# Kernel tuning notes

Hardware: AMD Instinct MI355X
Metric: run time of the kernel (lower is better)

The kernel has to match this reference:

```python
import jax, jax.numpy as jnp
import numpy as np

N = 100000
E = 1600000
C_IN = 128
H = 128
C_OUT = 128
DEPTH = 3
RATIO = 0.5
EPS = 1e-5


def gcn_conv(x, W, b, src, dst, mask, n):
    # PyG GCNConv: out = D^-1/2 (A+I) D^-1/2 (x @ W) + b, masked edges dropped
    h = x @ W  # [n, out]
    ew = mask.astype(h.dtype)  # [E]
    deg = 1.0 + jax.ops.segment_sum(ew, dst, num_segments=n)  # self-loop included
    dinv = jax.lax.rsqrt(deg)
    norm = dinv[src] * dinv[dst] * ew  # [E]
    agg = jax.ops.segment_sum(h[src] * norm[:, None], dst, num_segments=n)
    agg = agg + h * (1.0 / deg)[:, None]  # self-loop contribution
    return agg + b


def bn_train(x, g, beta):
    # BatchNorm1d training forward: biased variance over nodes
    m = jnp.mean(x, axis=0)
    v = jnp.mean((x - m) ** 2, axis=0)
    return (x - m) * jax.lax.rsqrt(v + EPS) * g + beta


def topk_pool(x, w, src, dst, mask, k):
    # score = tanh(x.w / ||w||); keep top-k nodes, relabel edges, mask invalid ones
    score = jnp.tanh((x * w).sum(-1) / jnp.sqrt((w * w).sum()))
    _, idx = jax.lax.top_k(score, k)
    n = x.shape[0]
    new_id = jnp.zeros((n,), jnp.int32).at[idx].set(jnp.arange(k, dtype=jnp.int32))
    kept = jnp.zeros((n,), bool).at[idx].set(True)
    mask2 = mask & kept[src] & kept[dst]
    return x[idx], new_id[src], new_id[dst], mask2, idx


def setup_inputs() -> dict:
    key = jax.random.key(0)
    ks = jax.random.split(key, 16)
    sc_in = 1.0 / np.sqrt(C_IN)
    sc_h = 1.0 / np.sqrt(H)
    sc_2h = 1.0 / np.sqrt(2 * H)
    return {
        "x": jax.random.normal(ks[0], (N, C_IN), jnp.float32),
        "edge_index": jax.random.randint(ks[1], (2, E), 0, N, dtype=jnp.int32),
        "in_W": jax.random.normal(ks[2], (C_IN, H), jnp.float32) * sc_in,
        "in_b": jnp.zeros((H,), jnp.float32),
        "dn_W": jax.random.normal(ks[3], (DEPTH, H, H), jnp.float32) * sc_h,
        "dn_b": jnp.zeros((DEPTH, H), jnp.float32),
        "dn_g": jnp.ones((DEPTH, H), jnp.float32),
        "dn_beta": jnp.zeros((DEPTH, H), jnp.float32),
        "pool_w": jax.random.normal(ks[4], (DEPTH, H), jnp.float32),
        "bot_W": jax.random.normal(ks[5], (H, H), jnp.float32) * sc_h,
        "bot_b": jnp.zeros((H,), jnp.float32),
        "up_W": jax.random.normal(ks[6], (DEPTH, 2 * H, H), jnp.float32) * sc_2h,
        "up_b": jnp.zeros((DEPTH, H), jnp.float32),
        "up_g": jnp.ones((DEPTH, H), jnp.float32),
        "up_beta": jnp.zeros((DEPTH, H), jnp.float32),
        "out_W": jax.random.normal(ks[7], (H, C_OUT), jnp.float32) * sc_h,
        "out_b": jnp.zeros((C_OUT,), jnp.float32),
    }


def reference(x, edge_index, in_W, in_b, dn_W, dn_b, dn_g, dn_beta, pool_w,
              bot_W, bot_b, up_W, up_b, up_g, up_beta, out_W, out_b):
    src, dst = edge_index[0], edge_index[1]
    mask = jnp.ones((src.shape[0],), bool)
    n = x.shape[0]
    x = gcn_conv(x, in_W, in_b, src, dst, mask, n)
    xs, stack = [], []
    for i in range(DEPTH):
        x = gcn_conv(x, dn_W[i], dn_b[i], src, dst, mask, n)
        x = jax.nn.relu(bn_train(x, dn_g[i], dn_beta[i]))
        xs.append(x)
        k = int(RATIO * n)
        x2, src2, dst2, mask2, idx = topk_pool(x, pool_w[i], src, dst, mask, k)
        stack.append((src, dst, mask, idx, n))
        x, src, dst, mask, n = x2, src2, dst2, mask2, k
    x = jax.nn.relu(gcn_conv(x, bot_W, bot_b, src, dst, mask, n))
    for i in range(DEPTH):
        psrc, pdst, pmask, idx, pn = stack[DEPTH - 1 - i]
        xf = jnp.zeros((pn, x.shape[1]), x.dtype).at[idx].set(x)  # unpool zero-scatter
        src, dst, mask, n = psrc, pdst, pmask, pn
        x = jnp.concatenate([xf, xs[DEPTH - 1 - i]], axis=1)  # [pn, 2H]
        x = gcn_conv(x, up_W[i], up_b[i], src, dst, mask, n)
        x = jax.nn.relu(bn_train(x, up_g[i], up_beta[i]))
    return gcn_conv(x, out_W, out_b, src, dst, mask, n)
```

## Files before the change

kernel.cpp:

```cpp
#include <hip/hip_runtime.h>

typedef unsigned long long ull;

#define N0_ 100000
#define N1_ 50000
#define N2_ 25000
#define N3_ 12500
#define EDG 1600000
#define CAP1 600000
#define CAP2 200000
#define CAP3 80000
#define RB 65536

struct Sel { ull prefix; int remaining; };


__global__ void sentinel_k(float* o, float v) { if (threadIdx.x == 0) o[0] = v; }

template <typename TA, typename TC, typename ACC>
__global__ __launch_bounds__(256) void matmul128(const TA* __restrict__ A,
    const float* __restrict__ W, const float* __restrict__ bias,
    TC* __restrict__ C, int n) {
  __shared__ float Al[64 * 33];
  __shared__ float Wl[32 * 128];
  int tid = threadIdx.x;
  int colb = tid & 31;
  int rg = tid >> 5;
  int row0 = blockIdx.x * 64;
  ACC acc[8][4];
#pragma unroll
  for (int r = 0; r < 8; ++r)
#pragma unroll
    for (int j = 0; j < 4; ++j) acc[r][j] = (ACC)0;
  for (int kt = 0; kt < 128; kt += 32) {
    for (int i = tid; i < 64 * 32; i += 256) {
      int r = i >> 5, kk = i & 31;
      int row = row0 + r;
      Al[r * 33 + kk] = (row < n) ? (float)A[(size_t)row * 128 + kt + kk] : 0.0f;
    }
    for (int i = tid; i < 32 * 128; i += 256) {
      int kk = i >> 7, c = i & 127;
      Wl[i] = W[(size_t)(kt + kk) * 128 + c];
    }
    __syncthreads();
#pragma unroll 4
    for (int kk = 0; kk < 32; ++kk) {
      ACC b0 = (ACC)Wl[kk * 128 + colb];
      ACC b1 = (ACC)Wl[kk * 128 + colb + 32];
      ACC b2 = (ACC)Wl[kk * 128 + colb + 64];
      ACC b3 = (ACC)Wl[kk * 128 + colb + 96];
#pragma unroll
      for (int r = 0; r < 8; ++r) {
        ACC a = (ACC)Al[(rg * 8 + r) * 33 + kk];
        acc[r][0] += a * b0; acc[r][1] += a * b1;
        acc[r][2] += a * b2; acc[r][3] += a * b3;
      }
    }
    __syncthreads();
  }
  ACC bb0 = 0, bb1 = 0, bb2 = 0, bb3 = 0;
  if (bias) {
    bb0 = (ACC)bias[colb]; bb1 = (ACC)bias[colb + 32];
    bb2 = (ACC)bias[colb + 64]; bb3 = (ACC)bias[colb + 96];
  }
  for (int r = 0; r < 8; ++r) {
    int row = row0 + rg * 8 + r;
    if (row < n) {
      size_t o = (size_t)row * 128 + colb;
      C[o] = (TC)(acc[r][0] + bb0); C[o + 32] = (TC)(acc[r][1] + bb1);
      C[o + 64] = (TC)(acc[r][2] + bb2); C[o + 96] = (TC)(acc[r][3] + bb3);
    }
  }
}

template <bool RELU>
__global__ __launch_bounds__(256) void agg_conv(const float* __restrict__ hp,
    const int* __restrict__ off, const int* __restrict__ csrc,
    const float* __restrict__ csrw,
    const double* __restrict__ dinv, const double* __restrict__ dgi,
    const float* __restrict__ bias, float* __restrict__ yp, int n) {
  const float4* __restrict__ h = (const float4*)hp;
  float4* __restrict__ y = (float4*)yp;
  int lane = threadIdx.x & 63;
  int c4 = lane & 31;
  int half = lane >> 5;
  int node = blockIdx.x * 4 + (threadIdx.x >> 6);
  if (node >= n) return;
  double di = dinv[node];
  double dg = dgi[node];
  double aX = 0, aY = 0, aZ = 0, aW = 0;
  int p0 = off[node], p1 = off[node + 1];
  int m = p1 - p0;
  int npair = m >> 1;
  int j = 0;
  for (; j + 8 <= npair; j += 8) {
    int e0 = p0 + 2 * j + half;
    int s0 = csrc[e0],      s1 = csrc[e0 + 2],  s2 = csrc[e0 + 4],  s3 = csrc[e0 + 6];
    int s4 = csrc[e0 + 8],  s5 = csrc[e0 + 10], s6 = csrc[e0 + 12], s7 = csrc[e0 + 14];
    double w0 = (double)csrw[e0],      w1 = (double)csrw[e0 + 2];
    double w2 = (double)csrw[e0 + 4],  w3 = (double)csrw[e0 + 6];
    double w4 = (double)csrw[e0 + 8],  w5 = (double)csrw[e0 + 10];
    double w6 = (double)csrw[e0 + 12], w7 = (double)csrw[e0 + 14];
    float4 v0 = h[(size_t)s0 * 32 + c4];
    float4 v1 = h[(size_t)s1 * 32 + c4];
    float4 v2 = h[(size_t)s2 * 32 + c4];
    float4 v3 = h[(size_t)s3 * 32 + c4];
    float4 v4 = h[(size_t)s4 * 32 + c4];
    float4 v5 = h[(size_t)s5 * 32 + c4];
    float4 v6 = h[(size_t)s6 * 32 + c4];
    float4 v7 = h[(size_t)s7 * 32 + c4];
    aX += (double)v0.x * w0; aY += (double)v0.y * w0;
    aZ += (double)v0.z * w0; aW += (double)v0.w * w0;
    aX += (double)v1.x * w1; aY += (double)v1.y * w1;
    aZ += (double)v1.z * w1; aW += (double)v1.w * w1;
    aX += (double)v2.x * w2; aY += (double)v2.y * w2;
    aZ += (double)v2.z * w2; aW += (double)v2.w * w2;
    aX += (double)v3.x * w3; aY += (double)v3.y * w3;
    aZ += (double)v3.z * w3; aW += (double)v3.w * w3;
    aX += (double)v4.x * w4; aY += (double)v4.y * w4;
    aZ += (double)v4.z * w4; aW += (double)v4.w * w4;
    aX += (double)v5.x * w5; aY += (double)v5.y * w5;
    aZ += (double)v5.z * w5; aW += (double)v5.w * w5;
    aX += (double)v6.x * w6; aY += (double)v6.y * w6;
    aZ += (double)v6.z * w6; aW += (double)v6.w * w6;
    aX += (double)v7.x * w7; aY += (double)v7.y * w7;
    aZ += (double)v7.z * w7; aW += (double)v7.w * w7;
  }
  for (; j + 4 <= npair; j += 4) {
    int e0 = p0 + 2 * j + half;
    int s0 = csrc[e0], s1 = csrc[e0 + 2], s2 = csrc[e0 + 4], s3 = csrc[e0 + 6];
    double w0 = (double)csrw[e0],     w1 = (double)csrw[e0 + 2];
    double w2 = (double)csrw[e0 + 4], w3 = (double)csrw[e0 + 6];
    float4 v0 = h[(size_t)s0 * 32 + c4];
    float4 v1 = h[(size_t)s1 * 32 + c4];
    float4 v2 = h[(size_t)s2 * 32 + c4];
    float4 v3 = h[(size_t)s3 * 32 + c4];
    aX += (double)v0.x * w0; aY += (double)v0.y * w0;
    aZ += (double)v0.z * w0; aW += (double)v0.w * w0;
    aX += (double)v1.x * w1; aY += (double)v1.y * w1;
    aZ += (double)v1.z * w1; aW += (double)v1.w * w1;
    aX += (double)v2.x * w2; aY += (double)v2.y * w2;
    aZ += (double)v2.z * w2; aW += (double)v2.w * w2;
    aX += (double)v3.x * w3; aY += (double)v3.y * w3;
    aZ += (double)v3.z * w3; aW += (double)v3.w * w3;
  }
  for (; j < npair; ++j) {
    int e = p0 + 2 * j + half;
    double w = (double)csrw[e];
    float4 v = h[(size_t)csrc[e] * 32 + c4];
    aX += (double)v.x * w; aY += (double)v.y * w;
    aZ += (double)v.z * w; aW += (double)v.w * w;
  }
  if ((m & 1) && half == 0) {
    int e = p1 - 1;
    double w = (double)csrw[e];
    float4 v = h[(size_t)csrc[e] * 32 + c4];
    aX += (double)v.x * w; aY += (double)v.y * w;
    aZ += (double)v.z * w; aW += (double)v.w * w;
  }
  double sX = aX + __shfl_xor(aX, 32);
  double sY = aY + __shfl_xor(aY, 32);
  double sZ = aZ + __shfl_xor(aZ, 32);
  double sW = aW + __shfl_xor(aW, 32);
  if (half == 0) {
    float4 hv = h[(size_t)node * 32 + c4];
    double bx = 0, by = 0, bz = 0, bw = 0;
    if (bias) {
      bx = (double)bias[c4 * 4 + 0]; by = (double)bias[c4 * 4 + 1];
      bz = (double)bias[c4 * 4 + 2]; bw = (double)bias[c4 * 4 + 3];
    }
    double rx = sX * di + (double)hv.x * dg + bx;
    double ry = sY * di + (double)hv.y * dg + by;
    double rz = sZ * di + (double)hv.z * dg + bz;
    double rw = sW * di + (double)hv.w * dg + bw;
    if (RELU) {
      rx = rx > 0.0 ? rx : 0.0; ry = ry > 0.0 ? ry : 0.0;
      rz = rz > 0.0 ? rz : 0.0; rw = rw > 0.0 ? rw : 0.0;
    }
    y[(size_t)node * 32 + c4] = make_float4((float)rx, (float)ry, (float)rz, (float)rw);
  }
}

__global__ void count_deg(const int* __restrict__ dst, int m, int* __restrict__ cnt) {
  int e = blockIdx.x * 256 + threadIdx.x;
  if (e < m) atomicAdd(&cnt[dst[e]], 1);
}

__global__ void fin_deg(const int* __restrict__ cnt, double* __restrict__ dinv,
                        double* __restrict__ dgi, int n) {
  int i = blockIdx.x * 256 + threadIdx.x;
  if (i < n) {
    double d = 1.0 + (double)cnt[i];
    dinv[i] = 1.0 / sqrt(d);
    dgi[i] = 1.0 / d;
  }
}

__global__ __launch_bounds__(256) void scan_part(const int* __restrict__ in,
                                                 int* __restrict__ bsum, int n) {
  __shared__ int ts[256];
  int base = blockIdx.x * 1024 + threadIdx.x * 4;
  int s = 0;
#pragma unroll
  for (int j = 0; j < 4; ++j) { int i = base + j; if (i < n) s += in[i]; }
  ts[threadIdx.x] = s;
  __syncthreads();
  for (int d = 128; d > 0; d >>= 1) {
    if (threadIdx.x < d) ts[threadIdx.x] += ts[threadIdx.x + d];
    __syncthreads();
  }
  if (threadIdx.x == 0) bsum[blockIdx.x] = ts[0];
}

__global__ __launch_bounds__(256) void scan_bsum(int* __restrict__ bsum, int nb) {
  __shared__ int ls[256];
  int t = threadIdx.x;
  int v = (t < nb) ? bsum[t] : 0;
  ls[t] = v;
  __syncthreads();
  for (int d = 1; d < 256; d <<= 1) {
    int u = (t >= d) ? ls[t - d] : 0;
    __syncthreads();
    ls[t] += u;
    __syncthreads();
  }
  if (t < nb) bsum[t] = ls[t] - v;
}

__global__ __launch_bounds__(256) void scan_out(const int* __restrict__ in,
    const int* __restrict__ bsum, int* __restrict__ out, int n, int nb) {
  __shared__ int ts[256];
  int base = blockIdx.x * 1024 + threadIdx.x * 4;
  int loc[4];
  int s = 0;
#pragma unroll
  for (int j = 0; j < 4; ++j) {
    int i = base + j;
    int v = (i < n) ? in[i] : 0;
    loc[j] = s; s += v;
  }
  ts[threadIdx.x] = s;
  __syncthreads();
  int mine = s;
  for (int d = 1; d < 256; d <<= 1) {
    int u = (threadIdx.x >= d) ? ts[threadIdx.x - d] : 0;
    __syncthreads();
    ts[threadIdx.x] += u;
    __syncthreads();
  }
  int toff = bsum[blockIdx.x] + ts[threadIdx.x] - mine;
#pragma unroll
  for (int j = 0; j < 4; ++j) {
    int i = base + j;
    if (i < n) out[i] = toff + loc[j];
  }
  if (blockIdx.x == nb - 1 && threadIdx.x == 255) out[n] = bsum[blockIdx.x] + ts[255];
}

template <int MODE>
__device__ __forceinline__ int sel_flag(ull u, ull pref, int epre, int rem) {
  if (MODE == 1) return (u == pref) ? 1 : 0;
  return (u > pref || (u == pref && epre < rem)) ? 1 : 0;
}

template <int MODE>
__global__ __launch_bounds__(256) void fscan_part(const ull* __restrict__ keys,
    const int* __restrict__ eqpre, const Sel* __restrict__ sel,
    int* __restrict__ bsum, int n) {
  __shared__ int ts[256];
  ull pref = sel->prefix;
  int rem = sel->remaining;
  int base = blockIdx.x * 1024 + threadIdx.x * 4;
  int s = 0;
#pragma unroll
  for (int j = 0; j < 4; ++j) {
    int i = base + j;
    if (i < n) s += sel_flag<MODE>(keys[i], pref, (MODE == 2) ? eqpre[i] : 0, rem);
  }
  ts[threadIdx.x] = s;
  __syncthreads();
  for (int d = 128; d > 0; d >>= 1) {
    if (threadIdx.x < d) ts[threadIdx.x] += ts[threadIdx.x + d];
    __syncthreads();
  }
  if (threadIdx.x == 0) bsum[blockIdx.x] = ts[0];
}

__global__ __launch_bounds__(256) void fscan_out1(const ull* __restrict__ keys,
    const Sel* __restrict__ sel, const int* __restrict__ bsum,
    int* __restrict__ eqpre_out, int n) {
  __shared__ int ts[256];
  ull pref = sel->prefix;
  int base = blockIdx.x * 1024 + threadIdx.x * 4;
  int loc[4];
  int s = 0;
#pragma unroll
  for (int j = 0; j < 4; ++j) {
    int i = base + j;
    int v = (i < n) ? sel_flag<1>(keys[i], pref, 0, 0) : 0;
    loc[j] = s; s += v;
  }
  ts[threadIdx.x] = s;
  __syncthreads();
  int mine = s;
  for (int d = 1; d < 256; d <<= 1) {
    int u = (threadIdx.x >= d) ? ts[threadIdx.x - d] : 0;
    __syncthreads();
    ts[threadIdx.x] += u;
    __syncthreads();
  }
  int toff = bsum[blockIdx.x] + ts[threadIdx.x] - mine;
#pragma unroll
  for (int j = 0; j < 4; ++j) {
    int i = base + j;
    if (i < n) eqpre_out[i] = toff + loc[j];
  }
}

__global__ __launch_bounds__(256) void fscan_out2(const ull* __restrict__ keys,
    const int* __restrict__ eqpre, const Sel* __restrict__ sel,
    const int* __restrict__ bsum, int* __restrict__ knid, int* __restrict__ idx,
    int n) {
  __shared__ int ts[256];
  ull pref = sel->prefix;
  int rem = sel->remaining;
  int base = blockIdx.x * 1024 + threadIdx.x * 4;
  int flg[4];
  int loc[4];
  int s = 0;
#pragma unroll
  for (int j = 0; j < 4; ++j) {
    int i = base + j;
    int v = (i < n) ? sel_flag<2>(keys[i], pref, eqpre[i], rem) : 0;
    flg[j] = v; loc[j] = s; s += v;
  }
  ts[threadIdx.x] = s;
  __syncthreads();
  int mine = s;
  for (int d = 1; d < 256; d <<= 1) {
    int u = (threadIdx.x >= d) ? ts[threadIdx.x - d] : 0;
    __syncthreads();
    ts[threadIdx.x] += u;
    __syncthreads();
  }
  int toff = bsum[blockIdx.x] + ts[threadIdx.x] - mine;
#pragma unroll
  for (int j = 0; j < 4; ++j) {
    int i = base + j;
    if (i < n) {
      if (flg[j]) {
        int nid = toff + loc[j];
        knid[i] = nid;
        idx[nid] = i;
      } else {
        knid[i] = -1;
      }
    }
  }
}

__global__ void csr_fill(const int* __restrict__ src, const int* __restrict__ dst,
                         int m, const int* __restrict__ off,
                         int* __restrict__ cursor, int* __restrict__ csrs,
                         float* __restrict__ csrw, const double* __restrict__ dinv) {
  int e = blockIdx.x * 256 + threadIdx.x;
  if (e < m) {
    int d = dst[e];
    int s = src[e];
    int pos = off[d] + atomicAdd(&cursor[d], 1);
    csrs[pos] = s;
    csrw[pos] = (float)dinv[s];
  }
}

__global__ void next_deg_fin(const int* __restrict__ off, const int* __restrict__ csrs,
                             const int* __restrict__ knid, int* __restrict__ ndeg,
                             double* __restrict__ ndinv, double* __restrict__ ndgi,
                             int n) {
  int d = blockIdx.x * 256 + threadIdx.x;
  if (d >= n) return;
  int nd = knid[d];
  if (nd < 0) return;
  int cnt = 0;
  int p1 = off[d + 1];
  for (int p = off[d]; p < p1; ++p) cnt += (knid[csrs[p]] >= 0) ? 1 : 0;
  ndeg[nd] = cnt;
  double dd = 1.0 + (double)cnt;
  ndinv[nd] = 1.0 / sqrt(dd);
  ndgi[nd] = 1.0 / dd;
}

__global__ void next_fill(const int* __restrict__ off, const int* __restrict__ csrs,
                          const int* __restrict__ knid, const int* __restrict__ noff,
                          const double* __restrict__ ndinv,
                          int* __restrict__ ncsrs, float* __restrict__ ncsrw, int n) {
  int d = blockIdx.x * 256 + threadIdx.x;
  if (d >= n) return;
  int nd = knid[d];
  if (nd < 0) return;
  int pos = noff[nd];
  int p1 = off[d + 1];
  for (int p = off[d]; p < p1; ++p) {
    int s = knid[csrs[p]];
    if (s >= 0) { ncsrs[pos] = s; ncsrw[pos] = (float)ndinv[s]; ++pos; }
  }
}

template <typename T>
__global__ __launch_bounds__(256) void bn_stats(const T* __restrict__ x, int n,
                                                double* __restrict__ part) {
  __shared__ double lsum[256], lsq[256];
  int c = threadIdx.x & 127, half = threadIdx.x >> 7;
  double s = 0, q = 0;
  for (int row = blockIdx.x * 2 + half; row < n; row += 512) {
    double v = (double)x[(size_t)row * 128 + c];
    s += v; q += v * v;
  }
  lsum[threadIdx.x] = s; lsq[threadIdx.x] = q;
  __syncthreads();
  if (half == 0) {
    part[blockIdx.x * 256 + c] = lsum[c] + lsum[c + 128];
    part[blockIdx.x * 256 + 128 + c] = lsq[c] + lsq[c + 128];
  }
}

__global__ void bn_final(const double* __restrict__ part, const float* __restrict__ g,
                         const float* __restrict__ beta, double invn,
                         double* __restrict__ ss) {
  int c = threadIdx.x;
  double s = 0, q = 0;
  for (int b = 0; b < 256; ++b) {
    s += part[b * 256 + c];
    q += part[b * 256 + 128 + c];
  }
  double m = s * invn;
  double v = q * invn - m * m;
  double sc = (double)g[c] / sqrt(v + 1e-5);
  ss[c] = sc;
  ss[128 + c] = (double)beta[c] - m * sc;
}

__global__ void bn_apply_relu4(const float4* __restrict__ x,
                               const double* __restrict__ ss,
                               float4* __restrict__ out, size_t total4) {
  size_t i = (size_t)blockIdx.x * 256 + threadIdx.x;
  if (i < total4) {
    int c0 = (int)((i & 31) * 4);
    float4 v = x[i];
    double r0 = (double)v.x * ss[c0 + 0] + ss[128 + c0 + 0];
    double r1 = (double)v.y * ss[c0 + 1] + ss[128 + c0 + 1];
    double r2 = (double)v.z * ss[c0 + 2] + ss[128 + c0 + 2];
    double r3 = (double)v.w * ss[c0 + 3] + ss[128 + c0 + 3];
    r0 = r0 > 0.0 ? r0 : 0.0; r1 = r1 > 0.0 ? r1 : 0.0;
    r2 = r2 > 0.0 ? r2 : 0.0; r3 = r3 > 0.0 ? r3 : 0.0;
    out[i] = make_float4((float)r0, (float)r1, (float)r2, (float)r3);
  }
}

__global__ void wnorm_k(const float* __restrict__ w, double* __restrict__ wn) {
  __shared__ double red[128];
  int c = threadIdx.x;
  double v = (double)w[c];
  red[c] = v * v;
  __syncthreads();
  for (int s = 64; s > 0; s >>= 1) { if (c < s) red[c] += red[c + s]; __syncthreads(); }
  if (c == 0) wn[0] = sqrt(red[0]);
}

__global__ __launch_bounds__(256) void score_key_k(const float* __restrict__ x,
    const float* __restrict__ w, const double* __restrict__ wn,
    ull* __restrict__ keys, int n) {
  __shared__ double red[256];
  int c = threadIdx.x & 127;
  int node = blockIdx.x * 2 + (threadIdx.x >> 7);
  double p = 0.0;
  if (node < n) p = (double)x[(size_t)node * 128 + c] * (double)w[c];
  red[threadIdx.x] = p;
  __syncthreads();
  for (int s = 64; s > 0; s >>= 1) {
    if (c < s) red[threadIdx.x] += red[threadIdx.x + s];
    __syncthreads();
  }
  if (c == 0 && node < n) {
    double sc = tanh(red[threadIdx.x] / wn[0]);
    ull u = (ull)__double_as_longlong(sc);
    u = (u >> 63) ? ~u : (u | 0x8000000000000000ULL);
    keys[node] = u;
  }
}

__global__ void rs_init(int* __restrict__ hist, Sel* sel, int k) {
  int i = blockIdx.x * 256 + threadIdx.x;
  if (i < 4 * RB) hist[i] = 0;
  if (i == 0) { sel->prefix = 0ULL; sel->remaining = k; }
}

__global__ void rs_hist16(const ull* __restrict__ keys, int n,
                          const Sel* __restrict__ sel, int shift, int pass,
                          int* __restrict__ hist) {
  int i = blockIdx.x * 256 + threadIdx.x;
  if (i < n) {
    ull k = keys[i];
    bool ok = (pass == 0) || (((k ^ sel->prefix) >> (shift + 16)) == 0);
    if (ok) atomicAdd(&hist[(int)((k >> shift) & 65535)], 1);
  }
}

__global__ __launch_bounds__(1024) void rs_pick16(const int* __restrict__ hist,
                                                  Sel* sel, int shift) {
  __shared__ int ls[1024];
  int t = threadIdx.x;
  int base = t * 64;
  int own = 0;
  for (int b = 0; b < 64; ++b) own += hist[base + b];
  ls[t] = own;
  __syncthreads();
  for (int d = 1; d < 1024; d <<= 1) {
    int v = (t + d < 1024) ? ls[t + d] : 0;
    __syncthreads();
    ls[t] += v;
    __syncthreads();
  }
  int rem = sel->remaining;
  int St = ls[t];
  int Snext = St - own;
  if (Snext < rem && rem <= St) {
    int cum = Snext;
    for (int b = 63; b >= 0; --b) {
      int c = hist[base + b];
      if (cum + c >= rem) {
        sel->prefix |= ((ull)(base + b)) << shift;
        sel->remaining = rem - cum;
        break;
      }
      cum += c;
    }
  }
}

__global__ void gather_rows4(const float4* __restrict__ xs, const int* __restrict__ idx,
                             float4* __restrict__ xo, int k) {
  int i = blockIdx.x * 256 + threadIdx.x;
  if (i < k * 32) xo[i] = xs[(size_t)idx[i >> 5] * 32 + (i & 31)];
}

__global__ void scatter_add_rows4(float4* __restrict__ h, const float4* __restrict__ t,
                                  const int* __restrict__ idx, int k) {
  int i = blockIdx.x * 256 + threadIdx.x;
  if (i < k * 32) {
    float4 a = h[(size_t)idx[i >> 5] * 32 + (i & 31)];
    float4 b = t[i];
    a.x += b.x; a.y += b.y; a.z += b.z; a.w += b.w;
    h[(size_t)idx[i >> 5] * 32 + (i & 31)] = a;
  }
}


extern "C" void kernel_launch(void* const* d_in, const int* in_sizes, int n_in,
                              void* d_out, int out_size, void* d_ws, size_t ws_size,
                              hipStream_t stream) {
  (void)in_sizes; (void)out_size;
  if (n_in < 17) return;
  const float* x_in   = (const float*)d_in[0];
  const int*   ei     = (const int*)  d_in[1];
  const float* in_W   = (const float*)d_in[2];
  const float* in_b   = (const float*)d_in[3];
  const float* dn_W   = (const float*)d_in[4];
  const float* dn_b   = (const float*)d_in[5];
  const float* dn_g   = (const float*)d_in[6];
  const float* dn_bt  = (const float*)d_in[7];
  const float* pool_w = (const float*)d_in[8];
  const float* bot_W  = (const float*)d_in[9];
  const float* bot_b  = (const float*)d_in[10];
  const float* up_W   = (const float*)d_in[11];
  const float* up_b   = (const float*)d_in[12];
  const float* up_g   = (const float*)d_in[13];
  const float* up_bt  = (const float*)d_in[14];
  const float* out_W  = (const float*)d_in[15];
  const float* out_b  = (const float*)d_in[16];
  float* outp = (float*)d_out;

  char* base = (char*)d_ws;
  size_t off = 0;
  auto alloc = [&](size_t b) -> void* {
    void* r = base + off;
    off = (off + b + 255) & ~(size_t)255;
    return r;
  };
  float* bufA = (float*)alloc((size_t)N0_ * 128 * 4);
  float* bufB = (float*)alloc((size_t)N0_ * 128 * 4);
  float* xs0f = (float*)alloc((size_t)N0_ * 128 * 4);
  float* xs1f = (float*)alloc((size_t)N1_ * 128 * 4);
  float* xs2f = (float*)alloc((size_t)N2_ * 128 * 4);

  int* csrs0 = (int*)alloc((size_t)EDG * 4);
  int* csrs1 = (int*)alloc((size_t)CAP1 * 4);
  int* csrs2 = (int*)alloc((size_t)CAP2 * 4);
  int* csrs3 = (int*)alloc((size_t)CAP3 * 4);
  float* csrw0 = (float*)alloc((size_t)EDG * 4);
  float* csrw1 = (float*)alloc((size_t)CAP1 * 4);
  float* csrw2 = (float*)alloc((size_t)CAP2 * 4);
  float* csrw3 = (float*)alloc((size_t)CAP3 * 4);
  int* csro0 = (int*)alloc((size_t)(N0_ + 1) * 4);
  int* csro1 = (int*)alloc((size_t)(N1_ + 1) * 4);
  int* csro2 = (int*)alloc((size_t)(N2_ + 1) * 4);
  int* csro3 = (int*)alloc((size_t)(N3_ + 1) * 4);
  double* dinv0 = (double*)alloc((size_t)N0_ * 8); double* dgi0 = (double*)alloc((size_t)N0_ * 8);
  double* dinv1 = (double*)alloc((size_t)N1_ * 8); double* dgi1 = (double*)alloc((size_t)N1_ * 8);
  double* dinv2 = (double*)alloc((size_t)N2_ * 8); double* dgi2 = (double*)alloc((size_t)N2_ * 8);
  double* dinv3 = (double*)alloc((size_t)N3_ * 8); double* dgi3 = (double*)alloc((size_t)N3_ * 8);
  ull* keys = (ull*)alloc((size_t)N0_ * 8);
  int* eqpre = (int*)alloc((size_t)(N0_ + 1) * 4);
  int* knid  = (int*)alloc((size_t)N0_ * 4);
  int* degcnt = (int*)alloc((size_t)N0_ * 4);
  int* cursor = (int*)alloc((size_t)N0_ * 4);
  int* idx0 = (int*)alloc((size_t)N1_ * 4);
  int* idx1 = (int*)alloc((size_t)N2_ * 4);
  int* idx2 = (int*)alloc((size_t)N3_ * 4);
  int* hist = (int*)alloc((size_t)4 * RB * 4);
  Sel* sel  = (Sel*)alloc(256);
  int* bscan = (int*)alloc(256 * 4);
  double* bns = (double*)alloc((size_t)256 * 256 * 8);
  double* ssb = (double*)alloc(256 * 8);
  double* wn  = (double*)alloc(256);
  if (off > ws_size) {
    sentinel_k<<<1, 64, 0, stream>>>(outp, (float)ws_size);
    return;
  }

  const int nL[4]   = {N0_, N1_, N2_, N3_};
  int* csrsL[4] = {csrs0, csrs1, csrs2, csrs3};
  float* csrwL[4] = {csrw0, csrw1, csrw2, csrw3};
  int* csroL[4] = {csro0, csro1, csro2, csro3};
  double* dinvL[4] = {dinv0, dinv1, dinv2, dinv3};
  double* dgiL[4]  = {dgi0, dgi1, dgi2, dgi3};
  int* idxL[3] = {idx0, idx1, idx2};

  auto cdiv = [](int a, int b) { return (a + b - 1) / b; };

  auto scan = [&](const int* in, int* out, int n) {
    int nb = cdiv(n, 1024);
    scan_part<<<nb, 256, 0, stream>>>(in, bscan, n);
    scan_bsum<<<1, 256, 0, stream>>>(bscan, nb);
    scan_out<<<nb, 256, 0, stream>>>(in, bscan, out, n, nb);
  };

  auto bn_f = [&](float* xp, int n, const float* g, const float* b, float* outb) {
    bn_stats<float><<<256, 256, 0, stream>>>(xp, n, bns);
    bn_final<<<1, 128, 0, stream>>>(bns, g, b, 1.0 / (double)n, ssb);
    bn_apply_relu4<<<cdiv(n * 32, 256), 256, 0, stream>>>(
        (const float4*)xp, ssb, (float4*)outb, (size_t)n * 32);
  };

  auto pool = [&](int i, const float* xcur, float* xnext) {
    int n = nL[i], k = nL[i + 1];
    int nb = cdiv(n, 1024);
    wnorm_k<<<1, 128, 0, stream>>>(pool_w + i * 128, wn);
    score_key_k<<<cdiv(n, 2), 256, 0, stream>>>(xcur, pool_w + i * 128, wn, keys, n);
    rs_init<<<1024, 256, 0, stream>>>(hist, sel, k);
    for (int p = 0; p < 4; ++p) {
      int shift = 48 - 16 * p;
      rs_hist16<<<cdiv(n, 256), 256, 0, stream>>>(keys, n, sel, shift, p, hist + p * RB);
      rs_pick16<<<1, 1024, 0, stream>>>(hist + p * RB, sel, shift);
    }
    fscan_part<1><<<nb, 256, 0, stream>>>(keys, nullptr, sel, bscan, n);
    scan_bsum<<<1, 256, 0, stream>>>(bscan, nb);
    fscan_out1<<<nb, 256, 0, stream>>>(keys, sel, bscan, eqpre, n);
    fscan_part<2><<<nb, 256, 0, stream>>>(keys, eqpre, sel, bscan, n);
    scan_bsum<<<1, 256, 0, stream>>>(bscan, nb);
    fscan_out2<<<nb, 256, 0, stream>>>(keys, eqpre, sel, bscan, knid, idxL[i], n);
    gather_rows4<<<cdiv(k * 32, 256), 256, 0, stream>>>(
        (const float4*)xcur, idxL[i], (float4*)xnext, k);
    next_deg_fin<<<cdiv(n, 256), 256, 0, stream>>>(csroL[i], csrsL[i], knid, degcnt,
                                                   dinvL[i + 1], dgiL[i + 1], n);
    scan(degcnt, csroL[i + 1], k);
    next_fill<<<cdiv(n, 256), 256, 0, stream>>>(csroL[i], csrsL[i], knid,
        csroL[i + 1], dinvL[i + 1], csrsL[i + 1], csrwL[i + 1], n);
  };

  hipMemsetAsync(degcnt, 0, (size_t)N0_ * 4, stream);
  count_deg<<<cdiv(EDG, 256), 256, 0, stream>>>(ei + EDG, EDG, degcnt);
  fin_deg<<<cdiv(N0_, 256), 256, 0, stream>>>(degcnt, dinv0, dgi0, N0_);
  scan(degcnt, csro0, N0_);
  hipMemsetAsync(cursor, 0, (size_t)N0_ * 4, stream);
  csr_fill<<<cdiv(EDG, 256), 256, 0, stream>>>(ei, ei + EDG, EDG, csro0, cursor,
                                               csrs0, csrw0, dinv0);

  agg_conv<false><<<cdiv(N0_, 4), 256, 0, stream>>>(
      x_in, csro0, csrs0, csrw0, dinv0, dgi0, nullptr, bufB, N0_);
  matmul128<float, float, double><<<cdiv(N0_, 64), 256, 0, stream>>>(bufB, in_W, in_b, bufA, N0_);

  matmul128<float, float, double><<<cdiv(N0_, 64), 256, 0, stream>>>(bufA, dn_W, nullptr, bufB, N0_);
  agg_conv<false><<<cdiv(N0_, 4), 256, 0, stream>>>(
      bufB, csro0, csrs0, csrw0, dinv0, dgi0, dn_b, bufA, N0_);
  bn_f(bufA, N0_, dn_g, dn_bt, xs0f);
  pool(0, xs0f, bufB);

  matmul128<float, float, double><<<cdiv(N1_, 64), 256, 0, stream>>>(bufB, dn_W + 16384, nullptr, bufA, N1_);
  agg_conv<false><<<cdiv(N1_, 4), 256, 0, stream>>>(
      bufA, csro1, csrs1, csrw1, dinv1, dgi1, dn_b + 128, bufB, N1_);
  bn_f(bufB, N1_, dn_g + 128, dn_bt + 128, xs1f);
  pool(1, xs1f, bufA);

  matmul128<float, float, double><<<cdiv(N2_, 64), 256, 0, stream>>>(bufA, dn_W + 32768, nullptr, bufB, N2_);
  agg_conv<false><<<cdiv(N2_, 4), 256, 0, stream>>>(
      bufB, csro2, csrs2, csrw2, dinv2, dgi2, dn_b + 256, bufA, N2_);
  bn_f(bufA, N2_, dn_g + 256, dn_bt + 256, xs2f);
  pool(2, xs2f, bufB);

  matmul128<float, float, double><<<cdiv(N3_, 64), 256, 0, stream>>>(bufB, bot_W, nullptr, bufA, N3_);
  float* zf = bufB;
  float* hf = bufA;
  float* tf = outp;
  agg_conv<true><<<cdiv(N3_, 4), 256, 0, stream>>>(
      bufA, csro3, csrs3, csrw3, dinv3, dgi3, bot_b, zf, N3_);

  for (int u = 0; u < 3; ++u) {
    int l = 2 - u;
    int nl = nL[l], nz = nL[l + 1];
    const float* Wt = up_W + u * 32768;
    const float* Wb = up_W + u * 32768 + 16384;
    const float* xsf = (u == 0) ? xs2f : (u == 1) ? xs1f : xs0f;
    matmul128<float, float, float><<<cdiv(nz, 64), 256, 0, stream>>>(zf, Wt, nullptr, tf, nz);
    matmul128<float, float, float><<<cdiv(nl, 64), 256, 0, stream>>>(xsf, Wb, nullptr, hf, nl);
    scatter_add_rows4<<<cdiv(nz * 32, 256), 256, 0, stream>>>(
        (float4*)hf, (const float4*)tf, idxL[l], nz);
    agg_conv<false><<<cdiv(nl, 4), 256, 0, stream>>>(
        hf, csroL[l], csrsL[l], csrwL[l], dinvL[l], dgiL[l], up_b + u * 128, zf, nl);
    bn_f(zf, nl, up_g + u * 128, up_bt + u * 128, zf);
  }

  matmul128<float, float, float><<<cdiv(N0_, 64), 256, 0, stream>>>(zf, out_W, nullptr, hf, N0_);
  agg_conv<false><<<cdiv(N0_, 4), 256, 0, stream>>>(
      hf, csro0, csrs0, csrw0, dinv0, dgi0, out_b, outp, N0_);
}
```

Measured before the change: 2.565 ms.

## Fuse BN-apply with pool scoring, merge top-k compaction scans, fuse unpool scatter-add

```diff
diff --git a/kernel.cpp b/kernel.cpp
--- a/kernel.cpp
+++ b/kernel.cpp
@@ -69,6 +69,56 @@
       size_t o = (size_t)row * 128 + colb;
       C[o] = (TC)(acc[r][0] + bb0); C[o + 32] = (TC)(acc[r][1] + bb1);
       C[o + 64] = (TC)(acc[r][2] + bb2); C[o + 96] = (TC)(acc[r][3] + bb3);
+    }
+  }
+}
+
+__global__ __launch_bounds__(256) void matmul128_sadd(const float* __restrict__ A,
+    const float* __restrict__ W, const int* __restrict__ idx,
+    float* __restrict__ C, int n) {
+  __shared__ float Al[64 * 33];
+  __shared__ float Wl[32 * 128];
+  int tid = threadIdx.x;
+  int colb = tid & 31;
+  int rg = tid >> 5;
+  int row0 = blockIdx.x * 64;
+  float acc[8][4];
+#pragma unroll
+  for (int r = 0; r < 8; ++r)
+#pragma unroll
+    for (int j = 0; j < 4; ++j) acc[r][j] = 0.0f;
+  for (int kt = 0; kt < 128; kt += 32) {
+    for (int i = tid; i < 64 * 32; i += 256) {
+      int r = i >> 5, kk = i & 31;
+      int row = row0 + r;
+      Al[r * 33 + kk] = (row < n) ? A[(size_t)row * 128 + kt + kk] : 0.0f;
+    }
+    for (int i = tid; i < 32 * 128; i += 256) {
+      int kk = i >> 7, c = i & 127;
+      Wl[i] = W[(size_t)(kt + kk) * 128 + c];
+    }
+    __syncthreads();
+#pragma unroll 4
+    for (int kk = 0; kk < 32; ++kk) {
+      float b0 = Wl[kk * 128 + colb];
+      float b1 = Wl[kk * 128 + colb + 32];
+      float b2 = Wl[kk * 128 + colb + 64];
+      float b3 = Wl[kk * 128 + colb + 96];
+#pragma unroll
+      for (int r = 0; r < 8; ++r) {
+        float a = Al[(rg * 8 + r) * 33 + kk];
+        acc[r][0] += a * b0; acc[r][1] += a * b1;
+        acc[r][2] += a * b2; acc[r][3] += a * b3;
+      }
+    }
+    __syncthreads();
+  }
+  for (int r = 0; r < 8; ++r) {
+    int row = row0 + rg * 8 + r;
+    if (row < n) {
+      size_t o = (size_t)idx[row] * 128 + colb;
+      C[o] += acc[r][0]; C[o + 32] += acc[r][1];
+      C[o + 64] += acc[r][2]; C[o + 96] += acc[r][3];
     }
   }
 }
@@ -257,99 +307,88 @@
   if (blockIdx.x == nb - 1 && threadIdx.x == 255) out[n] = bsum[blockIdx.x] + ts[255];
 }
 
-template <int MODE>
-__device__ __forceinline__ int sel_flag(ull u, ull pref, int epre, int rem) {
-  if (MODE == 1) return (u == pref) ? 1 : 0;
-  return (u > pref || (u == pref && epre < rem)) ? 1 : 0;
-}
-
-template <int MODE>
-__global__ __launch_bounds__(256) void fscan_part(const ull* __restrict__ keys,
-    const int* __restrict__ eqpre, const Sel* __restrict__ sel,
-    int* __restrict__ bsum, int n) {
-  __shared__ int ts[256];
+__global__ __launch_bounds__(256) void dsel_part(const ull* __restrict__ keys,
+    const Sel* __restrict__ sel, int2* __restrict__ bsum, int n) {
+  __shared__ int tg[256], te[256];
+  ull pref = sel->prefix;
+  int base = blockIdx.x * 1024 + threadIdx.x * 4;
+  int g = 0, e = 0;
+#pragma unroll
+  for (int j = 0; j < 4; ++j) {
+    int i = base + j;
+    if (i < n) {
+      ull u = keys[i];
+      g += (u > pref) ? 1 : 0;
+      e += (u == pref) ? 1 : 0;
+    }
+  }
+  tg[threadIdx.x] = g; te[threadIdx.x] = e;
+  __syncthreads();
+  for (int d = 128; d > 0; d >>= 1) {
+    if (threadIdx.x < d) { tg[threadIdx.x] += tg[threadIdx.x + d]; te[threadIdx.x] += te[threadIdx.x + d]; }
+    __syncthreads();
+  }
+  if (threadIdx.x == 0) bsum[blockIdx.x] = make_int2(tg[0], te[0]);
+}
+
+__global__ __launch_bounds__(256) void dsel_mid(int2* __restrict__ bsum, int nb) {
+  __shared__ int lg[256], le[256];
+  int t = threadIdx.x;
+  int2 v = (t < nb) ? bsum[t] : make_int2(0, 0);
+  lg[t] = v.x; le[t] = v.y;
+  __syncthreads();
+  for (int d = 1; d < 256; d <<= 1) {
+    int u1 = (t >= d) ? lg[t - d] : 0;
+    int u2 = (t >= d) ? le[t - d] : 0;
+    __syncthreads();
+    lg[t] += u1; le[t] += u2;
+    __syncthreads();
+  }
+  if (t < nb) bsum[t] = make_int2(lg[t] - v.x, le[t] - v.y);
+}
+
+__global__ __launch_bounds__(256) void dsel_out(const ull* __restrict__ keys,
+    const Sel* __restrict__ sel, const int2* __restrict__ bsum,
+    int* __restrict__ knid, int* __restrict__ idx, int n) {
+  __shared__ int tg[256], te[256];
   ull pref = sel->prefix;
   int rem = sel->remaining;
   int base = blockIdx.x * 1024 + threadIdx.x * 4;
-  int s = 0;
+  int gflg[4], eflg[4], gloc[4], eloc[4];
+  int g = 0, e = 0;
 #pragma unroll
   for (int j = 0; j < 4; ++j) {
     int i = base + j;
-    if (i < n) s += sel_flag<MODE>(keys[i], pref, (MODE == 2) ? eqpre[i] : 0, rem);
-  }
-  ts[threadIdx.x] = s;
-  __syncthreads();
-  for (int d = 128; d > 0; d >>= 1) {
-    if (threadIdx.x < d) ts[threadIdx.x] += ts[threadIdx.x + d];
-    __syncthreads();
-  }
-  if (threadIdx.x == 0) bsum[blockIdx.x] = ts[0];
-}
-
-__global__ __launch_bounds__(256) void fscan_out1(const ull* __restrict__ keys,
-    const Sel* __restrict__ sel, const int* __restrict__ bsum,
-    int* __restrict__ eqpre_out, int n) {
-  __shared__ int ts[256];
-  ull pref = sel->prefix;
-  int base = blockIdx.x * 1024 + threadIdx.x * 4;
-  int loc[4];
-  int s = 0;
-#pragma unroll
-  for (int j = 0; j < 4; ++j) {
-    int i = base + j;
-    int v = (i < n) ? sel_flag<1>(keys[i], pref, 0, 0) : 0;
-    loc[j] = s; s += v;
-  }
-  ts[threadIdx.x] = s;
-  __syncthreads();
-  int mine = s;
+    int gf = 0, ef = 0;
+    if (i < n) {
+      ull u = keys[i];
+      gf = (u > pref) ? 1 : 0;
+      ef = (u == pref) ? 1 : 0;
+    }
+    gflg[j] = gf; eflg[j] = ef; gloc[j] = g; eloc[j] = e;
+    g += gf; e += ef;
+  }
+  tg[threadIdx.x] = g; te[threadIdx.x] = e;
+  __syncthreads();
+  int gm = g, em = e;
   for (int d = 1; d < 256; d <<= 1) {
-    int u = (threadIdx.x >= d) ? ts[threadIdx.x - d] : 0;
-    __syncthreads();
-    ts[threadIdx.x] += u;
-    __syncthreads();
-  }
-  int toff = bsum[blockIdx.x] + ts[threadIdx.x] - mine;
-#pragma unroll
-  for (int j = 0; j < 4; ++j) {
-    int i = base + j;
-    if (i < n) eqpre_out[i] = toff + loc[j];
-  }
-}
-
-__global__ __launch_bounds__(256) void fscan_out2(const ull* __restrict__ keys,
-    const int* __restrict__ eqpre, const Sel* __restrict__ sel,
-    const int* __restrict__ bsum, int* __restrict__ knid, int* __restrict__ idx,
-    int n) {
-  __shared__ int ts[256];
-  ull pref = sel->prefix;
-  int rem = sel->remaining;
-  int base = blockIdx.x * 1024 + threadIdx.x * 4;
-  int flg[4];
-  int loc[4];
-  int s = 0;
-#pragma unroll
-  for (int j = 0; j < 4; ++j) {
-    int i = base + j;
-    int v = (i < n) ? sel_flag<2>(keys[i], pref, eqpre[i], rem) : 0;
-    flg[j] = v; loc[j] = s; s += v;
-  }
-  ts[threadIdx.x] = s;
-  __syncthreads();
-  int mine = s;
-  for (int d = 1; d < 256; d <<= 1) {
-    int u = (threadIdx.x >= d) ? ts[threadIdx.x - d] : 0;
-    __syncthreads();
-    ts[threadIdx.x] += u;
-    __syncthreads();
-  }
-  int toff = bsum[blockIdx.x] + ts[threadIdx.x] - mine;
+    int u1 = (threadIdx.x >= d) ? tg[threadIdx.x - d] : 0;
+    int u2 = (threadIdx.x >= d) ? te[threadIdx.x - d] : 0;
+    __syncthreads();
+    tg[threadIdx.x] += u1; te[threadIdx.x] += u2;
+    __syncthreads();
+  }
+  int2 bo = bsum[blockIdx.x];
+  int goff = bo.x + tg[threadIdx.x] - gm;
+  int eoff = bo.y + te[threadIdx.x] - em;
 #pragma unroll
   for (int j = 0; j < 4; ++j) {
     int i = base + j;
     if (i < n) {
-      if (flg[j]) {
-        int nid = toff + loc[j];
+      int gp = goff + gloc[j];
+      int ep = eoff + eloc[j];
+      if (gflg[j] || (eflg[j] && ep < rem)) {
+        int nid = gp + (ep < rem ? ep : rem);
         knid[i] = nid;
         idx[nid] = i;
       } else {
@@ -440,9 +479,8 @@
   ss[128 + c] = (double)beta[c] - m * sc;
 }
 
-__global__ void bn_apply_relu4(const float4* __restrict__ x,
-                               const double* __restrict__ ss,
-                               float4* __restrict__ out, size_t total4) {
+__global__ void bn_apply_relu4(float4* __restrict__ x, const double* __restrict__ ss,
+                               size_t total4) {
   size_t i = (size_t)blockIdx.x * 256 + threadIdx.x;
   if (i < total4) {
     int c0 = (int)((i & 31) * 4);
@@ -453,46 +491,57 @@
     double r3 = (double)v.w * ss[c0 + 3] + ss[128 + c0 + 3];
     r0 = r0 > 0.0 ? r0 : 0.0; r1 = r1 > 0.0 ? r1 : 0.0;
     r2 = r2 > 0.0 ? r2 : 0.0; r3 = r3 > 0.0 ? r3 : 0.0;
-    out[i] = make_float4((float)r0, (float)r1, (float)r2, (float)r3);
-  }
-}
-
-__global__ void wnorm_k(const float* __restrict__ w, double* __restrict__ wn) {
-  __shared__ double red[128];
-  int c = threadIdx.x;
-  double v = (double)w[c];
-  red[c] = v * v;
-  __syncthreads();
-  for (int s = 64; s > 0; s >>= 1) { if (c < s) red[c] += red[c + s]; __syncthreads(); }
-  if (c == 0) wn[0] = sqrt(red[0]);
-}
-
-__global__ __launch_bounds__(256) void score_key_k(const float* __restrict__ x,
-    const float* __restrict__ w, const double* __restrict__ wn,
-    ull* __restrict__ keys, int n) {
-  __shared__ double red[256];
-  int c = threadIdx.x & 127;
-  int node = blockIdx.x * 2 + (threadIdx.x >> 7);
-  double p = 0.0;
-  if (node < n) p = (double)x[(size_t)node * 128 + c] * (double)w[c];
-  red[threadIdx.x] = p;
+    x[i] = make_float4((float)r0, (float)r1, (float)r2, (float)r3);
+  }
+}
+
+__global__ __launch_bounds__(256) void bn_score_k(const float4* __restrict__ x,
+    const double* __restrict__ ss, float4* __restrict__ snap,
+    const float* __restrict__ w, ull* __restrict__ keys, int n,
+    int nodeBlocks, int* __restrict__ hist, Sel* sel, int k) {
+  if ((int)blockIdx.x >= nodeBlocks) {
+    int i = (blockIdx.x - nodeBlocks) * 256 + threadIdx.x;
+    if (i < 4 * RB) hist[i] = 0;
+    if (i == 0) { sel->prefix = 0ULL; sel->remaining = k; }
+    return;
+  }
+  __shared__ double wsh[128];
+  __shared__ double wnv;
+  int tid = threadIdx.x;
+  if (tid < 128) wsh[tid] = (double)w[tid] * (double)w[tid];
   __syncthreads();
   for (int s = 64; s > 0; s >>= 1) {
-    if (c < s) red[threadIdx.x] += red[threadIdx.x + s];
-    __syncthreads();
-  }
-  if (c == 0 && node < n) {
-    double sc = tanh(red[threadIdx.x] / wn[0]);
+    if (tid < s) wsh[tid] += wsh[tid + s];
+    __syncthreads();
+  }
+  if (tid == 0) wnv = sqrt(wsh[0]);
+  __syncthreads();
+  int c4 = tid & 31;
+  int node = blockIdx.x * 8 + (tid >> 5);
+  if (node >= n) return;
+  float4 v = x[(size_t)node * 32 + c4];
+  int c0 = c4 * 4;
+  double r0 = (double)v.x * ss[c0 + 0] + ss[128 + c0 + 0];
+  double r1 = (double)v.y * ss[c0 + 1] + ss[128 + c0 + 1];
+  double r2 = (double)v.z * ss[c0 + 2] + ss[128 + c0 + 2];
+  double r3 = (double)v.w * ss[c0 + 3] + ss[128 + c0 + 3];
+  r0 = r0 > 0.0 ? r0 : 0.0; r1 = r1 > 0.0 ? r1 : 0.0;
+  r2 = r2 > 0.0 ? r2 : 0.0; r3 = r3 > 0.0 ? r3 : 0.0;
+  float4 o = make_float4((float)r0, (float)r1, (float)r2, (float)r3);
+  snap[(size_t)node * 32 + c4] = o;
+  double p = (double)o.x * (double)w[c0 + 0] + (double)o.y * (double)w[c0 + 1]
+           + (double)o.z * (double)w[c0 + 2] + (double)o.w * (double)w[c0 + 3];
+  p += __shfl_xor(p, 1);
+  p += __shfl_xor(p, 2);
+  p += __shfl_xor(p, 4);
+  p += __shfl_xor(p, 8);
+  p += __shfl_xor(p, 16);
+  if (c4 == 0) {
+    double sc = tanh(p / wnv);
     ull u = (ull)__double_as_longlong(sc);
     u = (u >> 63) ? ~u : (u | 0x8000000000000000ULL);
     keys[node] = u;
   }
-}
-
-__global__ void rs_init(int* __restrict__ hist, Sel* sel, int k) {
-  int i = blockIdx.x * 256 + threadIdx.x;
-  if (i < 4 * RB) hist[i] = 0;
-  if (i == 0) { sel->prefix = 0ULL; sel->remaining = k; }
 }
 
 __global__ void rs_hist16(const ull* __restrict__ keys, int n,
@@ -542,17 +591,6 @@
                              float4* __restrict__ xo, int k) {
   int i = blockIdx.x * 256 + threadIdx.x;
   if (i < k * 32) xo[i] = xs[(size_t)idx[i >> 5] * 32 + (i & 31)];
-}
-
-__global__ void scatter_add_rows4(float4* __restrict__ h, const float4* __restrict__ t,
-                                  const int* __restrict__ idx, int k) {
-  int i = blockIdx.x * 256 + threadIdx.x;
-  if (i < k * 32) {
-    float4 a = h[(size_t)idx[i >> 5] * 32 + (i & 31)];
-    float4 b = t[i];
-    a.x += b.x; a.y += b.y; a.z += b.z; a.w += b.w;
-    h[(size_t)idx[i >> 5] * 32 + (i & 31)] = a;
-  }
 }
 
 
@@ -610,7 +648,6 @@
   double* dinv2 = (double*)alloc((size_t)N2_ * 8); double* dgi2 = (double*)alloc((size_t)N2_ * 8);
   double* dinv3 = (double*)alloc((size_t)N3_ * 8); double* dgi3 = (double*)alloc((size_t)N3_ * 8);
   ull* keys = (ull*)alloc((size_t)N0_ * 8);
-  int* eqpre = (int*)alloc((size_t)(N0_ + 1) * 4);
   int* knid  = (int*)alloc((size_t)N0_ * 4);
   int* degcnt = (int*)alloc((size_t)N0_ * 4);
   int* cursor = (int*)alloc((size_t)N0_ * 4);
@@ -619,10 +656,9 @@
   int* idx2 = (int*)alloc((size_t)N3_ * 4);
   int* hist = (int*)alloc((size_t)4 * RB * 4);
   Sel* sel  = (Sel*)alloc(256);
-  int* bscan = (int*)alloc(256 * 4);
+  int* bscan = (int*)alloc(256 * 8);
   double* bns = (double*)alloc((size_t)256 * 256 * 8);
   double* ssb = (double*)alloc(256 * 8);
-  double* wn  = (double*)alloc(256);
   if (off > ws_size) {
     sentinel_k<<<1, 64, 0, stream>>>(outp, (float)ws_size);
     return;
@@ -645,30 +681,33 @@
     scan_out<<<nb, 256, 0, stream>>>(in, bscan, out, n, nb);
   };
 
-  auto bn_f = [&](float* xp, int n, const float* g, const float* b, float* outb) {
+  auto bn_score = [&](float* xp, int n, const float* g, const float* b,
+                      float* snap, const float* pw, int k) {
+    bn_stats<float><<<256, 256, 0, stream>>>(xp, n, bns);
+    bn_final<<<1, 128, 0, stream>>>(bns, g, b, 1.0 / (double)n, ssb);
+    int nodeBlocks = cdiv(n, 8);
+    bn_score_k<<<nodeBlocks + 1024, 256, 0, stream>>>(
+        (const float4*)xp, ssb, (float4*)snap, pw, keys, n, nodeBlocks, hist, sel, k);
+  };
+
+  auto bn_up = [&](float* xp, int n, const float* g, const float* b) {
     bn_stats<float><<<256, 256, 0, stream>>>(xp, n, bns);
     bn_final<<<1, 128, 0, stream>>>(bns, g, b, 1.0 / (double)n, ssb);
     bn_apply_relu4<<<cdiv(n * 32, 256), 256, 0, stream>>>(
-        (const float4*)xp, ssb, (float4*)outb, (size_t)n * 32);
+        (float4*)xp, ssb, (size_t)n * 32);
   };
 
   auto pool = [&](int i, const float* xcur, float* xnext) {
     int n = nL[i], k = nL[i + 1];
     int nb = cdiv(n, 1024);
-    wnorm_k<<<1, 128, 0, stream>>>(pool_w + i * 128, wn);
-    score_key_k<<<cdiv(n, 2), 256, 0, stream>>>(xcur, pool_w + i * 128, wn, keys, n);
-    rs_init<<<1024, 256, 0, stream>>>(hist, sel, k);
     for (int p = 0; p < 4; ++p) {
       int shift = 48 - 16 * p;
       rs_hist16<<<cdiv(n, 256), 256, 0, stream>>>(keys, n, sel, shift, p, hist + p * RB);
       rs_pick16<<<1, 1024, 0, stream>>>(hist + p * RB, sel, shift);
     }
-    fscan_part<1><<<nb, 256, 0, stream>>>(keys, nullptr, sel, bscan, n);
-    scan_bsum<<<1, 256, 0, stream>>>(bscan, nb);
-    fscan_out1<<<nb, 256, 0, stream>>>(keys, sel, bscan, eqpre, n);
-    fscan_part<2><<<nb, 256, 0, stream>>>(keys, eqpre, sel, bscan, n);
-    scan_bsum<<<1, 256, 0, stream>>>(bscan, nb);
-    fscan_out2<<<nb, 256, 0, stream>>>(keys, eqpre, sel, bscan, knid, idxL[i], n);
+    dsel_part<<<nb, 256, 0, stream>>>(keys, sel, (int2*)bscan, n);
+    dsel_mid<<<1, 256, 0, stream>>>((int2*)bscan, nb);
+    dsel_out<<<nb, 256, 0, stream>>>(keys, sel, (int2*)bscan, knid, idxL[i], n);
     gather_rows4<<<cdiv(k * 32, 256), 256, 0, stream>>>(
         (const float4*)xcur, idxL[i], (float4*)xnext, k);
     next_deg_fin<<<cdiv(n, 256), 256, 0, stream>>>(csroL[i], csrsL[i], knid, degcnt,
@@ -693,25 +732,24 @@
   matmul128<float, float, double><<<cdiv(N0_, 64), 256, 0, stream>>>(bufA, dn_W, nullptr, bufB, N0_);
   agg_conv<false><<<cdiv(N0_, 4), 256, 0, stream>>>(
       bufB, csro0, csrs0, csrw0, dinv0, dgi0, dn_b, bufA, N0_);
-  bn_f(bufA, N0_, dn_g, dn_bt, xs0f);
+  bn_score(bufA, N0_, dn_g, dn_bt, xs0f, pool_w, N1_);
   pool(0, xs0f, bufB);
 
   matmul128<float, float, double><<<cdiv(N1_, 64), 256, 0, stream>>>(bufB, dn_W + 16384, nullptr, bufA, N1_);
   agg_conv<false><<<cdiv(N1_, 4), 256, 0, stream>>>(
       bufA, csro1, csrs1, csrw1, dinv1, dgi1, dn_b + 128, bufB, N1_);
-  bn_f(bufB, N1_, dn_g + 128, dn_bt + 128, xs1f);
+  bn_score(bufB, N1_, dn_g + 128, dn_bt + 128, xs1f, pool_w + 128, N2_);
   pool(1, xs1f, bufA);
 
   matmul128<float, float, double><<<cdiv(N2_, 64), 256, 0, stream>>>(bufA, dn_W + 32768, nullptr, bufB, N2_);
   agg_conv<false><<<cdiv(N2_, 4), 256, 0, stream>>>(
       bufB, csro2, csrs2, csrw2, dinv2, dgi2, dn_b + 256, bufA, N2_);
-  bn_f(bufA, N2_, dn_g + 256, dn_bt + 256, xs2f);
+  bn_score(bufA, N2_, dn_g + 256, dn_bt + 256, xs2f, pool_w + 256, N3_);
   pool(2, xs2f, bufB);
 
   matmul128<float, float, double><<<cdiv(N3_, 64), 256, 0, stream>>>(bufB, bot_W, nullptr, bufA, N3_);
   float* zf = bufB;
   float* hf = bufA;
-  float* tf = outp;
   agg_conv<true><<<cdiv(N3_, 4), 256, 0, stream>>>(
       bufA, csro3, csrs3, csrw3, dinv3, dgi3, bot_b, zf, N3_);
 
@@ -721,13 +759,11 @@
     const float* Wt = up_W + u * 32768;
     const float* Wb = up_W + u * 32768 + 16384;
     const float* xsf = (u == 0) ? xs2f : (u == 1) ? xs1f : xs0f;
-    matmul128<float, float, float><<<cdiv(nz, 64), 256, 0, stream>>>(zf, Wt, nullptr, tf, nz);
     matmul128<float, float, float><<<cdiv(nl, 64), 256, 0, stream>>>(xsf, Wb, nullptr, hf, nl);
-    scatter_add_rows4<<<cdiv(nz * 32, 256), 256, 0, stream>>>(
-        (float4*)hf, (const float4*)tf, idxL[l], nz);
+    matmul128_sadd<<<cdiv(nz, 64), 256, 0, stream>>>(zf, Wt, idxL[l], hf, nz);
     agg_conv<false><<<cdiv(nl, 4), 256, 0, stream>>>(
         hf, csroL[l], csrsL[l], csrwL[l], dinvL[l], dgiL[l], up_b + u * 128, zf, nl);
-    bn_f(zf, nl, up_g + u * 128, up_bt + u * 128, zf);
+    bn_up(zf, nl, up_g + u * 128, up_bt + u * 128);
   }
 
   matmul128<float, float, float><<<cdiv(N0_, 64), 256, 0, stream>>>(zf, out_W, nullptr, hf, N0_);
```

Measured after the change: 2.453 ms. 4.4% less time.
